# Optimization experiments

Hardware: AMD Instinct MI355X
Metric: run time of the kernel (lower is better)

Reference implementation:

```python
import jax, jax.numpy as jnp
import numpy as np

NU = 100000  # user nodes
NI = 100000  # item nodes
NE = 600000  # edges per etype


def mean_agg(Wh, src, dst, n_dst):
    # copy_u + mean reduce: gather projected src feats, segment-mean over dst
    msg = Wh[src]                                               # [E, d]
    s = jax.ops.segment_sum(msg, dst, num_segments=n_dst)       # [n_dst, d]
    deg = jax.ops.segment_sum(jnp.ones((src.shape[0],), Wh.dtype), dst,
                              num_segments=n_dst)               # [n_dst]
    return s / jnp.maximum(deg, 1.0)[:, None]                   # isolated nodes -> 0


def setup_inputs() -> dict:
    key = jax.random.key(0)
    ks = jax.random.split(key, 20)
    d_in, d_hid, d_out = 128, 128, 16
    inp = {
        'embed_user': jax.random.normal(ks[0], (NU, d_in), jnp.float32),
        'embed_item': jax.random.normal(ks[1], (NI, d_in), jnp.float32),
        'src_uu': jax.random.randint(ks[2], (NE,), 0, NU, jnp.int32),
        'dst_uu': jax.random.randint(ks[3], (NE,), 0, NU, jnp.int32),
        'src_ui': jax.random.randint(ks[4], (NE,), 0, NU, jnp.int32),
        'dst_ui': jax.random.randint(ks[5], (NE,), 0, NI, jnp.int32),
        'src_iu': jax.random.randint(ks[6], (NE,), 0, NI, jnp.int32),
        'dst_iu': jax.random.randint(ks[7], (NE,), 0, NU, jnp.int32),
        'W0_uu': jax.random.normal(ks[8], (d_in, d_hid), jnp.float32) * 0.05,
        'b0_uu': jax.random.normal(ks[9], (d_hid,), jnp.float32) * 0.05,
        'W0_ui': jax.random.normal(ks[10], (d_in, d_hid), jnp.float32) * 0.05,
        'b0_ui': jax.random.normal(ks[11], (d_hid,), jnp.float32) * 0.05,
        'W0_iu': jax.random.normal(ks[12], (d_in, d_hid), jnp.float32) * 0.05,
        'b0_iu': jax.random.normal(ks[13], (d_hid,), jnp.float32) * 0.05,
        'W1_uu': jax.random.normal(ks[14], (d_hid, d_out), jnp.float32) * 0.05,
        'b1_uu': jax.random.normal(ks[15], (d_out,), jnp.float32) * 0.05,
        'W1_ui': jax.random.normal(ks[16], (d_hid, d_out), jnp.float32) * 0.05,
        'b1_ui': jax.random.normal(ks[17], (d_out,), jnp.float32) * 0.05,
        'W1_iu': jax.random.normal(ks[18], (d_hid, d_out), jnp.float32) * 0.05,
        'b1_iu': jax.random.normal(ks[19], (d_out,), jnp.float32) * 0.05,
    }
    return inp


def reference(embed_user, embed_item,
              src_uu, dst_uu, src_ui, dst_ui, src_iu, dst_iu,
              W0_uu, b0_uu, W0_ui, b0_ui, W0_iu, b0_iu,
              W1_uu, b1_uu, W1_ui, b1_ui, W1_iu, b1_iu):
    # Layer 0: per-etype linear, copy_u+mean per etype, sum-combine per dst ntype
    h_user = (mean_agg(embed_user @ W0_uu + b0_uu, src_uu, dst_uu, NU)
              + mean_agg(embed_item @ W0_iu + b0_iu, src_iu, dst_iu, NU))
    h_item = mean_agg(embed_user @ W0_ui + b0_ui, src_ui, dst_ui, NI)
    h_user = jax.nn.relu(h_user)
    h_item = jax.nn.relu(h_item)
    # Layer 1 (dropout p=0): only category='user' output is returned
    out = (mean_agg(h_user @ W1_uu + b1_uu, src_uu, dst_uu, NU)
           + mean_agg(h_item @ W1_iu + b1_iu, src_iu, dst_iu, NU))
    return out
```

## Files before the change

kernel.cpp:

```cpp
#include <hip/hip_runtime.h>
#include <hip/hip_bf16.h>

#define NU 100000
#define NI 100000
#define NEDGE 600000
#define DIN 128
#define DOUT 16
#define NPAD 100032
#define BSH 9
#define NBUCK 196
#define NSB 256
#define SCH 2344

typedef __attribute__((ext_vector_type(8))) short short8;
typedef __attribute__((ext_vector_type(4))) float f32x4;

#define W_EU   0ull
#define W_AUI  6400000ull
#define W_AUU  12802048ull
#define W_AIU  19204096ull
#define W_PW   25606144ull
#define W_OFFU 25632768ull
#define W_OFFI 25732784ull
#define W_OFFX 25832800ull
#define W_SUU  25932816ull
#define W_SIU  26532816ull
#define W_SUI  27132816ull
#define W_EI   27732944ull
#define WS_FULL_BYTES (34132944ull * 4)

__device__ inline unsigned pack_bf16(float x, float y) {
  __hip_bfloat162 h = __float22bfloat162_rn(make_float2(x, y));
  unsigned u;
  __builtin_memcpy(&u, &h, 4);
  return u;
}

__device__ inline short bf16_bits(float x) {
  __hip_bfloat16 h = __float2bfloat16(x);
  short s;
  __builtin_memcpy(&s, &h, 2);
  return s;
}

__device__ inline void bf2_accw(unsigned u, float w, float& ax, float& ay) {
  unsigned lo = u << 16, hi = u & 0xffff0000u;
  float f0, f1;
  __builtin_memcpy(&f0, &lo, 4);
  __builtin_memcpy(&f1, &hi, 4);
  ax = fmaf(f0, w, ax);
  ay = fmaf(f1, w, ay);
}

__global__ __launch_bounds__(256) void prep_kernel(
    const float* __restrict__ Eu, const float* __restrict__ Ei,
    unsigned* __restrict__ Eu_b, unsigned* __restrict__ Ei_b,
    const int* __restrict__ d_uu, const int* __restrict__ d_iu, const int* __restrict__ d_ui,
    int* __restrict__ M,
    const float* __restrict__ W0_uu, const float* __restrict__ W0_ui,
    const float* __restrict__ W0_iu, const float* __restrict__ W1_uu,
    const float* __restrict__ W1_iu, short* __restrict__ pW0_uu, short* __restrict__ pW0_ui,
    short* __restrict__ pW0_iu, short* __restrict__ pW1_uu, short* __restrict__ pW1_iu,
    int nconvU, int nconvI) {
  __shared__ int h[NBUCK];
  int b = blockIdx.x;
  int tid = threadIdx.x;
  if (b < nconvU + nconvI) {
    const float* src;
    unsigned* dst;
    int t;
    if (b < nconvU) { src = Eu; dst = Eu_b; t = b * 256 + tid; }
    else { src = Ei; dst = Ei_b; t = (b - nconvU) * 256 + tid; }
    const float4* s4 = (const float4*)src;
    float4 x = s4[(size_t)t * 2], y = s4[(size_t)t * 2 + 1];
    uint4 o;
    o.x = pack_bf16(x.x, x.y);
    o.y = pack_bf16(x.z, x.w);
    o.z = pack_bf16(y.x, y.y);
    o.w = pack_bf16(y.z, y.w);
    ((uint4*)dst)[t] = o;
    return;
  }
  b -= nconvU + nconvI;
  if (b < 3 * NSB) {
    int t = b / NSB, k = b % NSB;
    if (tid < NBUCK) h[tid] = 0;
    __syncthreads();
    const int* d = (t == 0) ? d_uu : (t == 1) ? d_iu : d_ui;
    int e0 = k * SCH, e1 = min(e0 + SCH, NEDGE);
    for (int e = e0 + tid; e < e1; e += 256) atomicAdd(&h[d[e] >> BSH], 1);
    __syncthreads();
    if (tid < NBUCK) M[t * (NBUCK * NSB) + tid * NSB + k] = h[tid];
    return;
  }
  b -= 3 * NSB;
  int t = b * 256 + tid;
  const float* src;
  short* dst;
  int base;
  bool w1 = false;
  if (t < 16384) { src = W0_uu; dst = pW0_uu; base = t; }
  else if (t < 32768) { src = W0_ui; dst = pW0_ui; base = t - 16384; }
  else if (t < 49152) { src = W0_iu; dst = pW0_iu; base = t - 32768; }
  else if (t < 51200) { src = W1_uu; dst = pW1_uu; base = t - 49152; w1 = true; }
  else if (t < 53248) { src = W1_iu; dst = pW1_iu; base = t - 51200; w1 = true; }
  else return;
  int j = base & 7;
  int lane = (base >> 3) & 63;
  int frag = base >> 9;
  int quad = lane >> 4, l16 = lane & 15;
  float val;
  if (!w1) {
    int kc = frag >> 3, nt = frag & 7;
    val = src[(kc * 32 + quad * 8 + j) * 128 + nt * 16 + l16];
  } else {
    int kc = frag;
    val = src[(kc * 32 + quad * 8 + j) * 16 + l16];
  }
  dst[base] = bf16_bits(val);
}

__global__ __launch_bounds__(256) void scanM_kernel(int* __restrict__ M,
                                                    int* __restrict__ Btot) {
  int t = blockIdx.x / NBUCK, b = blockIdx.x % NBUCK;
  int* Mt = M + t * (NBUCK * NSB) + b * NSB;
  __shared__ int wls[4];
  __shared__ int tot;
  int tid = threadIdx.x, lane = tid & 63, wv = tid >> 6;
  int v = Mt[tid];
  int x = v;
#pragma unroll
  for (int d = 1; d < 64; d <<= 1) {
    int y = __shfl_up(x, d, 64);
    if (lane >= d) x += y;
  }
  if (lane == 63) wls[wv] = x;
  __syncthreads();
  if (tid == 0) {
    int r = 0;
#pragma unroll
    for (int i = 0; i < 4; i++) { int tt = wls[i]; wls[i] = r; r += tt; }
    tot = r;
  }
  __syncthreads();
  Mt[tid] = x - v + wls[wv];
  if (tid == 0) Btot[t * NBUCK + b] = tot;
}

__global__ __launch_bounds__(256) void scanB_kernel(const int* __restrict__ Btot,
                                                    int* __restrict__ Bbase) {
  int t = blockIdx.x;
  __shared__ int wls[4];
  int tid = threadIdx.x, lane = tid & 63, wv = tid >> 6;
  int v = (tid < NBUCK) ? Btot[t * NBUCK + tid] : 0;
  int x = v;
#pragma unroll
  for (int d = 1; d < 64; d <<= 1) {
    int y = __shfl_up(x, d, 64);
    if (lane >= d) x += y;
  }
  if (lane == 63) wls[wv] = x;
  __syncthreads();
  if (tid == 0) {
    int r = 0;
#pragma unroll
    for (int i = 0; i < 4; i++) { int tt = wls[i]; wls[i] = r; r += tt; }
  }
  __syncthreads();
  if (tid < NBUCK) Bbase[t * NBUCK + tid] = x - v + wls[wv];
}

__global__ __launch_bounds__(256) void coarse_scatter_kernel(
    const int* __restrict__ s_uu, const int* __restrict__ d_uu,
    const int* __restrict__ s_iu, const int* __restrict__ d_iu,
    const int* __restrict__ s_ui, const int* __restrict__ d_ui,
    const int* __restrict__ M, const int* __restrict__ Bbase, uint2* __restrict__ pairs) {
  __shared__ int cur[NBUCK];
  int t = blockIdx.x / NSB, k = blockIdx.x % NSB;
  int tid = threadIdx.x;
  if (tid < NBUCK) cur[tid] = M[t * (NBUCK * NSB) + tid * NSB + k] + Bbase[t * NBUCK + tid];
  __syncthreads();
  const int* src = (t == 0) ? s_uu : (t == 1) ? s_iu : s_ui;
  const int* dst = (t == 0) ? d_uu : (t == 1) ? d_iu : d_ui;
  uint2* pr = pairs + (size_t)t * NEDGE;
  int e0 = k * SCH, e1 = min(e0 + SCH, NEDGE);
  for (int e = e0 + tid; e < e1; e += 256) {
    int d = dst[e];
    int pos = atomicAdd(&cur[d >> BSH], 1);
    pr[pos] = make_uint2((unsigned)src[e], (unsigned)d);
  }
}

__global__ __launch_bounds__(256) void fine_sort_kernel(
    const uint2* __restrict__ pairs, const int* __restrict__ Bbase,
    const int* __restrict__ Btot,
    int* __restrict__ off_uu, int* __restrict__ off_iu, int* __restrict__ off_ui,
    int* __restrict__ ssrc_uu, int* __restrict__ ssrc_iu, int* __restrict__ ssrc_ui) {
  __shared__ int h[1 << BSH];
  __shared__ int wls[4];
  int t = blockIdx.x / NBUCK, b = blockIdx.x % NBUCK;
  int tid = threadIdx.x, lane = tid & 63, wv = tid >> 6;
  int* off = (t == 0) ? off_uu : (t == 1) ? off_iu : off_ui;
  int* ss = (t == 0) ? ssrc_uu : (t == 1) ? ssrc_iu : ssrc_ui;
  const uint2* pr = pairs + (size_t)t * NEDGE;
  int base = b << BSH;
  int base_off = Bbase[t * NBUCK + b];
  int cnt = Btot[t * NBUCK + b];
  h[tid] = 0;
  h[tid + 256] = 0;
  __syncthreads();
  for (int e = base_off + tid; e < base_off + cnt; e += 256)
    atomicAdd(&h[(int)pr[e].y - base], 1);
  __syncthreads();
  int h0 = h[2 * tid], h1 = h[2 * tid + 1];
  int s = h0 + h1, x = s;
#pragma unroll
  for (int d = 1; d < 64; d <<= 1) {
    int y = __shfl_up(x, d, 64);
    if (lane >= d) x += y;
  }
  if (lane == 63) wls[wv] = x;
  __syncthreads();
  if (tid == 0) {
    int r = 0;
#pragma unroll
    for (int i = 0; i < 4; i++) { int tt = wls[i]; wls[i] = r; r += tt; }
  }
  __syncthreads();
  int excl = base_off + x - s + wls[wv];
  h[2 * tid] = excl;
  h[2 * tid + 1] = excl + h0;
  __syncthreads();
  int nn = min(1 << BSH, NU - base);
  for (int i = tid; i < nn; i += 256) off[base + i] = h[i];
  if (b == NBUCK - 1 && tid == 0) off[NU] = base_off + cnt;
  __syncthreads();
  for (int e = base_off + tid; e < base_off + cnt; e += 256) {
    uint2 p = pr[e];
    int pos = atomicAdd(&h[(int)p.y - base], 1);
    ss[pos] = (int)p.x;
  }
}

__global__ __launch_bounds__(64, 4) void fused_layer_kernel(
    const uint4* __restrict__ Xu4, const void* __restrict__ Xi, int xi_bf16,
    const int* __restrict__ off_ui, const int* __restrict__ off_uu, const int* __restrict__ off_iu,
    const int* __restrict__ s_ui, const int* __restrict__ s_uu, const int* __restrict__ s_iu,
    const short* __restrict__ pW0_ui, const short* __restrict__ pW0_uu,
    const short* __restrict__ pW0_iu, const float* __restrict__ b0_ui,
    const float* __restrict__ b0_uu, const float* __restrict__ b0_iu,
    const short* __restrict__ pW1_iu, const short* __restrict__ pW1_uu,
    const float* __restrict__ b1_iu, const float* __restrict__ b1_uu,
    float* __restrict__ P_iu, float* __restrict__ P_uu, int nbi) {
  __shared__ __align__(16) float hs[2560];

  const int lane = threadIdx.x;
  const bool user = (int)blockIdx.x >= nbi;
  const int blk = user ? (int)blockIdx.x - nbi : (int)blockIdx.x;
  const int rb = blk * 16;

  float* hw = &hs[0];
  uint4* A0 = (uint4*)hw;
  uint4* A1 = A0 + 256;

  {
    const int g = lane >> 4, l16 = lane & 15;
    const int npass = user ? 2 : 1;
#pragma unroll 1
    for (int pass = 0; pass < npass; pass++) {
      const int* off = pass ? off_iu : (user ? off_uu : off_ui);
      const int* ss = pass ? s_iu : (user ? s_uu : s_ui);
      uint4* A = pass ? A1 : A0;
      const bool bf = pass ? (xi_bf16 != 0) : true;
      const uint4* X = pass ? (const uint4*)Xi : Xu4;
      const float4* Xf = (const float4*)Xi;
      if (bf) {
#pragma unroll 1
        for (int ip = 0; ip < 2; ip++) {
          int rA = g * 4 + ip * 2, rB = rA + 1;
          int nodeA = rb + rA, nodeB = rb + rB;
          float acA[8], acB[8];
#pragma unroll
          for (int j = 0; j < 8; j++) { acA[j] = 0.f; acB[j] = 0.f; }
          int s0A = 0, s1A = 0, s0B = 0, s1B = 0;
          if (nodeA < NU) { s0A = off[nodeA]; s1A = off[nodeA + 1]; }
          if (nodeB < NU) { s0B = off[nodeB]; s1B = off[nodeB + 1]; }
          int degA = s1A - s0A, degB = s1B - s0B;
#pragma unroll 1
          for (int eA = s0A, eB = s0B; eA < s1A || eB < s1B; eA += 8, eB += 8) {
            int idxA[8], idxB[8];
            float wtA[8], wtB[8];
#pragma unroll
            for (int j = 0; j < 8; j++) {
              int ea = eA + j, eb = eB + j;
              wtA[j] = (ea < s1A) ? 1.f : 0.f;
              wtB[j] = (eb < s1B) ? 1.f : 0.f;
              idxA[j] = ss[max(min(ea, s1A - 1), 0)];
              idxB[j] = ss[max(min(eb, s1B - 1), 0)];
            }
            uint4 vA[8], vB[8];
#pragma unroll
            for (int j = 0; j < 8; j++) vA[j] = X[(size_t)idxA[j] * 16 + l16];
#pragma unroll
            for (int j = 0; j < 8; j++) vB[j] = X[(size_t)idxB[j] * 16 + l16];
#pragma unroll
            for (int j = 0; j < 8; j++) {
              bf2_accw(vA[j].x, wtA[j], acA[0], acA[1]);
              bf2_accw(vA[j].y, wtA[j], acA[2], acA[3]);
              bf2_accw(vA[j].z, wtA[j], acA[4], acA[5]);
              bf2_accw(vA[j].w, wtA[j], acA[6], acA[7]);
            }
#pragma unroll
            for (int j = 0; j < 8; j++) {
              bf2_accw(vB[j].x, wtB[j], acB[0], acB[1]);
              bf2_accw(vB[j].y, wtB[j], acB[2], acB[3]);
              bf2_accw(vB[j].z, wtB[j], acB[4], acB[5]);
              bf2_accw(vB[j].w, wtB[j], acB[6], acB[7]);
            }
          }
          float invA = 1.0f / fmaxf((float)degA, 1.0f);
          float invB = 1.0f / fmaxf((float)degB, 1.0f);
          uint4 oA, oB;
          oA.x = pack_bf16(acA[0] * invA, acA[1] * invA);
          oA.y = pack_bf16(acA[2] * invA, acA[3] * invA);
          oA.z = pack_bf16(acA[4] * invA, acA[5] * invA);
          oA.w = pack_bf16(acA[6] * invA, acA[7] * invA);
          oB.x = pack_bf16(acB[0] * invB, acB[1] * invB);
          oB.y = pack_bf16(acB[2] * invB, acB[3] * invB);
          oB.z = pack_bf16(acB[4] * invB, acB[5] * invB);
          oB.w = pack_bf16(acB[6] * invB, acB[7] * invB);
          A[rA * 16 + (l16 ^ (rA & 7))] = oA;
          A[rB * 16 + (l16 ^ (rB & 7))] = oB;
        }
      } else {
#pragma unroll 1
        for (int it = 0; it < 4; it++) {
          int r = g * 4 + it;
          int node = rb + r;
          float ac[8];
#pragma unroll
          for (int j = 0; j < 8; j++) ac[j] = 0.f;
          int deg = 0;
          if (node < NU) {
            int s0 = off[node], s1 = off[node + 1];
            deg = s1 - s0;
            if (deg > 0) {
              for (int e = s0; e < s1; e += 4) {
                int idx[4];
                float wt[4];
#pragma unroll
                for (int j = 0; j < 4; j++) {
                  int ee = e + j;
                  bool v = ee < s1;
                  idx[j] = ss[v ? ee : s1 - 1];
                  wt[j] = v ? 1.f : 0.f;
                }
#pragma unroll
                for (int j = 0; j < 4; j++) {
                  float4 pa = Xf[(size_t)idx[j] * 32 + l16 * 2];
                  float4 qa = Xf[(size_t)idx[j] * 32 + l16 * 2 + 1];
                  ac[0] = fmaf(pa.x, wt[j], ac[0]); ac[1] = fmaf(pa.y, wt[j], ac[1]);
                  ac[2] = fmaf(pa.z, wt[j], ac[2]); ac[3] = fmaf(pa.w, wt[j], ac[3]);
                  ac[4] = fmaf(qa.x, wt[j], ac[4]); ac[5] = fmaf(qa.y, wt[j], ac[5]);
                  ac[6] = fmaf(qa.z, wt[j], ac[6]); ac[7] = fmaf(qa.w, wt[j], ac[7]);
                }
              }
            }
          }
          float inv = 1.0f / fmaxf((float)deg, 1.0f);
          uint4 o;
          o.x = pack_bf16(ac[0] * inv, ac[1] * inv);
          o.y = pack_bf16(ac[2] * inv, ac[3] * inv);
          o.z = pack_bf16(ac[4] * inv, ac[5] * inv);
          o.w = pack_bf16(ac[6] * inv, ac[7] * inv);
          A[r * 16 + (l16 ^ (r & 7))] = o;
        }
      }
    }
  }
  __syncthreads();

  const int quad = lane >> 4, q16 = lane & 15;
  const int* off0 = user ? off_uu : off_ui;
  const short* W0a = user ? pW0_uu : pW0_ui;
  const float* b0a = user ? b0_uu : b0_ui;
  const short* W1p = user ? pW1_uu : pW1_iu;
  const float* b1v = user ? b1_uu : b1_iu;
  float* P = user ? P_uu : P_iu;

  float m0[4], m1[4];
#pragma unroll
  for (int r = 0; r < 4; r++) {
    int rr = rb + quad * 4 + r;
    m0[r] = 0.f;
    m1[r] = 0.f;
    if (rr < NU) {
      m0[r] = (off0[rr + 1] > off0[rr]) ? 1.f : 0.f;
      if (user) m1[r] = (off_iu[rr + 1] > off_iu[rr]) ? 1.f : 0.f;
    }
  }

  f32x4 acc[8];
#pragma unroll
  for (int nt = 0; nt < 8; nt++) {
    float ba = b0a[nt * 16 + q16];
    float bb = user ? b0_iu[nt * 16 + q16] : 0.f;
#pragma unroll
    for (int r = 0; r < 4; r++) acc[nt][r] = ba * m0[r] + bb * m1[r];
  }

  const short8* B0p = (const short8*)W0a;
  const short8* B1p = (const short8*)pW0_iu;
  union u4s8 { uint4 u; short8 s; };
#pragma unroll
  for (int kc = 0; kc < 4; kc++) {
    int c = kc * 4 + quad;
    u4s8 a0, a1;
    a0.u = A0[q16 * 16 + (c ^ (q16 & 7))];
    if (user) a1.u = A1[q16 * 16 + (c ^ (q16 & 7))];
#pragma unroll
    for (int nt = 0; nt < 8; nt++) {
      short8 b0 = B0p[(kc * 8 + nt) * 64 + lane];
      acc[nt] = __builtin_amdgcn_mfma_f32_16x16x32_bf16(a0.s, b0, acc[nt], 0, 0, 0);
      if (user) {
        short8 bb = B1p[(kc * 8 + nt) * 64 + lane];
        acc[nt] = __builtin_amdgcn_mfma_f32_16x16x32_bf16(a1.s, bb, acc[nt], 0, 0, 0);
      }
    }
  }
  __syncthreads();

#pragma unroll
  for (int nt = 0; nt < 8; nt++) {
    int col = nt * 16 + q16;
    float4 v;
    v.x = fmaxf(acc[nt][0], 0.f);
    v.y = fmaxf(acc[nt][1], 0.f);
    v.z = fmaxf(acc[nt][2], 0.f);
    v.w = fmaxf(acc[nt][3], 0.f);
    *(float4*)&hw[col * 20 + quad * 4] = v;
  }
  __syncthreads();

  f32x4 acc2;
  {
    float bv = b1v[q16];
    acc2[0] = bv; acc2[1] = bv; acc2[2] = bv; acc2[3] = bv;
  }
  const short8* W1f = (const short8*)W1p;
#pragma unroll
  for (int kc = 0; kc < 4; kc++) {
    float f[8];
#pragma unroll
    for (int j = 0; j < 8; j++) f[j] = hw[(kc * 32 + quad * 8 + j) * 20 + q16];
    union { uint4 u; short8 s; } hf;
    hf.u.x = pack_bf16(f[0], f[1]);
    hf.u.y = pack_bf16(f[2], f[3]);
    hf.u.z = pack_bf16(f[4], f[5]);
    hf.u.w = pack_bf16(f[6], f[7]);
    short8 bw = W1f[kc * 64 + lane];
    acc2 = __builtin_amdgcn_mfma_f32_16x16x32_bf16(hf.s, bw, acc2, 0, 0, 0);
  }
#pragma unroll
  for (int r = 0; r < 4; r++) {
    int rr = rb + quad * 4 + r;
    if (rr < NU) P[(size_t)rr * DOUT + q16] = acc2[r];
  }
}

__global__ __launch_bounds__(256) void out_kernel(const float4* __restrict__ P_uu,
                                                  const float4* __restrict__ P_iu,
                                                  const int* __restrict__ off_uu,
                                                  const int* __restrict__ s_uu,
                                                  const int* __restrict__ off_iu,
                                                  const int* __restrict__ s_iu,
                                                  float4* __restrict__ out) {
  int w = threadIdx.x >> 6, lane = threadIdx.x & 63;
  int q = lane & 3;
  int sl = (lane >> 2) & 3;
  int nl = lane >> 4;
  int node = blockIdx.x * 16 + w * 4 + nl;
  float4 a = make_float4(0.f, 0.f, 0.f, 0.f);
  float4 b = a;
  int s0 = off_uu[node], s1 = off_uu[node + 1];
  for (int e = s0 + sl; e < s1; e += 4) {
    float4 v = P_uu[(size_t)s_uu[e] * 4 + q];
    a.x += v.x; a.y += v.y; a.z += v.z; a.w += v.w;
  }
  int t0 = off_iu[node], t1 = off_iu[node + 1];
  for (int e = t0 + sl; e < t1; e += 4) {
    float4 v = P_iu[(size_t)s_iu[e] * 4 + q];
    b.x += v.x; b.y += v.y; b.z += v.z; b.w += v.w;
  }
  float ia = 1.0f / fmaxf((float)(s1 - s0), 1.0f);
  float ib = 1.0f / fmaxf((float)(t1 - t0), 1.0f);
  float4 r;
  r.x = a.x * ia + b.x * ib;
  r.y = a.y * ia + b.y * ib;
  r.z = a.z * ia + b.z * ib;
  r.w = a.w * ia + b.w * ib;
  r.x += __shfl_xor(r.x, 4, 64); r.y += __shfl_xor(r.y, 4, 64);
  r.z += __shfl_xor(r.z, 4, 64); r.w += __shfl_xor(r.w, 4, 64);
  r.x += __shfl_xor(r.x, 8, 64); r.y += __shfl_xor(r.y, 8, 64);
  r.z += __shfl_xor(r.z, 8, 64); r.w += __shfl_xor(r.w, 8, 64);
  if (sl == 0) out[(size_t)node * 4 + q] = r;
}

extern "C" void kernel_launch(void* const* d_in, const int* in_sizes, int n_in,
                              void* d_out, int out_size, void* d_ws, size_t ws_size,
                              hipStream_t stream) {
  (void)in_sizes; (void)n_in; (void)out_size;
  const float* embed_user = (const float*)d_in[0];
  const float* embed_item = (const float*)d_in[1];
  const int* src_uu = (const int*)d_in[2];
  const int* dst_uu = (const int*)d_in[3];
  const int* src_ui = (const int*)d_in[4];
  const int* dst_ui = (const int*)d_in[5];
  const int* src_iu = (const int*)d_in[6];
  const int* dst_iu = (const int*)d_in[7];
  const float* W0_uu = (const float*)d_in[8];
  const float* b0_uu = (const float*)d_in[9];
  const float* W0_ui = (const float*)d_in[10];
  const float* b0_ui = (const float*)d_in[11];
  const float* W0_iu = (const float*)d_in[12];
  const float* b0_iu = (const float*)d_in[13];
  const float* W1_uu = (const float*)d_in[14];
  const float* b1_uu = (const float*)d_in[15];
  const float* W1_iu = (const float*)d_in[18];
  const float* b1_iu = (const float*)d_in[19];
  float* out = (float*)d_out;

  char* ws = (char*)d_ws;
  unsigned* Eu_b = (unsigned*)(ws + W_EU * 4);
  short* pW0_uu = (short*)(ws + W_PW * 4);
  short* pW0_ui = pW0_uu + 16384;
  short* pW0_iu = pW0_uu + 32768;
  short* pW1_uu = pW0_uu + 49152;
  short* pW1_iu = pW0_uu + 51200;
  int* off_uu = (int*)(ws + W_OFFU * 4);
  int* off_iu = (int*)(ws + W_OFFI * 4);
  int* off_ui = (int*)(ws + W_OFFX * 4);
  int* ssrc_uu = (int*)(ws + W_SUU * 4);
  int* ssrc_iu = (int*)(ws + W_SIU * 4);
  int* ssrc_ui = (int*)(ws + W_SUI * 4);
  unsigned* Ei_b = (unsigned*)(ws + W_EI * 4);
  uint2* pairs = (uint2*)(ws + W_AUI * 4);
  int* M = (int*)(ws + W_AUU * 4);
  int* Btot = M + NBUCK * NSB * 3;
  int* Bbase = Btot + NBUCK * 3;
  float* P_iu = (float*)(ws + W_AUU * 4);
  float* P_uu = P_iu + 1600000;

  const int full = (ws_size >= WS_FULL_BYTES) ? 1 : 0;
  const int nconvU = 6250, nconvI = full ? 6250 : 0;
  const void* Xi = full ? (const void*)Ei_b : (const void*)embed_item;

  prep_kernel<<<nconvU + nconvI + 3 * NSB + 208, 256, 0, stream>>>(
      embed_user, embed_item, Eu_b, Ei_b, dst_uu, dst_iu, dst_ui, M,
      W0_uu, W0_ui, W0_iu, W1_uu, W1_iu, pW0_uu, pW0_ui, pW0_iu, pW1_uu, pW1_iu,
      nconvU, nconvI);

  scanM_kernel<<<3 * NBUCK, 256, 0, stream>>>(M, Btot);
  scanB_kernel<<<3, 256, 0, stream>>>(Btot, Bbase);
  coarse_scatter_kernel<<<3 * NSB, 256, 0, stream>>>(src_uu, dst_uu, src_iu, dst_iu,
                                                     src_ui, dst_ui, M, Bbase, pairs);
  fine_sort_kernel<<<3 * NBUCK, 256, 0, stream>>>(pairs, Bbase, Btot,
                                                  off_uu, off_iu, off_ui,
                                                  ssrc_uu, ssrc_iu, ssrc_ui);

  const int nbi = NPAD / 16;
  fused_layer_kernel<<<2 * nbi, 64, 0, stream>>>(
      (const uint4*)Eu_b, Xi, full, off_ui, off_uu, off_iu,
      ssrc_ui, ssrc_uu, ssrc_iu,
      pW0_ui, pW0_uu, pW0_iu, b0_ui, b0_uu, b0_iu,
      pW1_iu, pW1_uu, b1_iu, b1_uu, P_iu, P_uu, nbi);

  out_kernel<<<NU / 16, 256, 0, stream>>>((const float4*)P_uu, (const float4*)P_iu,
                                          off_uu, ssrc_uu, off_iu, ssrc_iu,
                                          (float4*)out);
}
```

Before: 345.7 us.

## Pack four waves per block and stage ReLU hidden tile as bf16 in LDS

The fused layer kernel now launches 256-thread blocks holding four independent waves, each owning its own 16-row tile and its own LDS slice, instead of one wave per block. This cuts block count and per-block scheduling overhead. The ReLU'd hidden activations are packed to bf16 pairs through a lane shuffle before being written to LDS, so the second MFMA stage reads one uint4 per lane instead of eight strided floats plus packing. The costs are more LDS per block (32 KB), which may limit occupancy, and block-wide __syncthreads that now couple four waves whose edge gather loads can differ.

```diff
diff --git a/kernel.cpp b/kernel.cpp
--- a/kernel.cpp
+++ b/kernel.cpp
@@ -242,7 +242,7 @@
   }
 }
 
-__global__ __launch_bounds__(64, 4) void fused_layer_kernel(
+__global__ __launch_bounds__(256, 4) void fused_layer_kernel(
     const uint4* __restrict__ Xu4, const void* __restrict__ Xi, int xi_bf16,
     const int* __restrict__ off_ui, const int* __restrict__ off_uu, const int* __restrict__ off_iu,
     const int* __restrict__ s_ui, const int* __restrict__ s_uu, const int* __restrict__ s_iu,
@@ -252,16 +252,18 @@
     const short* __restrict__ pW1_iu, const short* __restrict__ pW1_uu,
     const float* __restrict__ b1_iu, const float* __restrict__ b1_uu,
     float* __restrict__ P_iu, float* __restrict__ P_uu, int nbi) {
-  __shared__ __align__(16) float hs[2560];
-
-  const int lane = threadIdx.x;
+  __shared__ __align__(16) unsigned hs2[4][2048];
+
+  const int tid = threadIdx.x;
+  const int w = tid >> 6, lane = tid & 63;
   const bool user = (int)blockIdx.x >= nbi;
   const int blk = user ? (int)blockIdx.x - nbi : (int)blockIdx.x;
-  const int rb = blk * 16;
-
-  float* hw = &hs[0];
-  uint4* A0 = (uint4*)hw;
+  const int rb = blk * 64 + w * 16;
+
+  unsigned* base = hs2[w];
+  uint4* A0 = (uint4*)base;
   uint4* A1 = A0 + 256;
+  unsigned* h2 = base;
 
   {
     const int g = lane >> 4, l16 = lane & 15;
@@ -432,13 +434,14 @@
 
 #pragma unroll
   for (int nt = 0; nt < 8; nt++) {
-    int col = nt * 16 + q16;
-    float4 v;
-    v.x = fmaxf(acc[nt][0], 0.f);
-    v.y = fmaxf(acc[nt][1], 0.f);
-    v.z = fmaxf(acc[nt][2], 0.f);
-    v.w = fmaxf(acc[nt][3], 0.f);
-    *(float4*)&hw[col * 20 + quad * 4] = v;
+#pragma unroll
+    for (int r = 0; r < 4; r++) {
+      float v = fmaxf(acc[nt][r], 0.f);
+      float p = __shfl_xor(v, 1, 64);
+      if ((q16 & 1) == 0) {
+        h2[(quad * 4 + r) * 68 + nt * 8 + (q16 >> 1)] = pack_bf16(v, p);
+      }
+    }
   }
   __syncthreads();
 
@@ -448,16 +451,11 @@
     acc2[0] = bv; acc2[1] = bv; acc2[2] = bv; acc2[3] = bv;
   }
   const short8* W1f = (const short8*)W1p;
+  const uint4* h4 = (const uint4*)base;
 #pragma unroll
   for (int kc = 0; kc < 4; kc++) {
-    float f[8];
-#pragma unroll
-    for (int j = 0; j < 8; j++) f[j] = hw[(kc * 32 + quad * 8 + j) * 20 + q16];
-    union { uint4 u; short8 s; } hf;
-    hf.u.x = pack_bf16(f[0], f[1]);
-    hf.u.y = pack_bf16(f[2], f[3]);
-    hf.u.z = pack_bf16(f[4], f[5]);
-    hf.u.w = pack_bf16(f[6], f[7]);
+    u4s8 hf;
+    hf.u = h4[q16 * 17 + kc * 4 + quad];
     short8 bw = W1f[kc * 64 + lane];
     acc2 = __builtin_amdgcn_mfma_f32_16x16x32_bf16(hf.s, bw, acc2, 0, 0, 0);
   }
@@ -568,8 +566,8 @@
                                                   off_uu, off_iu, off_ui,
                                                   ssrc_uu, ssrc_iu, ssrc_ui);
 
-  const int nbi = NPAD / 16;
-  fused_layer_kernel<<<2 * nbi, 64, 0, stream>>>(
+  const int nbi = NPAD / 64;
+  fused_layer_kernel<<<2 * nbi, 256, 0, stream>>>(
       (const uint4*)Eu_b, Xi, full, off_ui, off_uu, off_iu,
       ssrc_ui, ssrc_uu, ssrc_iu,
       pW0_ui, pW0_uu, pW0_iu, b0_ui, b0_uu, b0_iu,
```

Result: slower. 362.4 us (+4.8%).
